# Performance work log

Hardware: AMD Instinct MI355X
Metric: run time of the kernel (lower is better)

Reference implementation:

```python
import jax, jax.numpy as jnp
import numpy as np

N_NODES = 50000
N_EDGES = 600000
IN_DIM = 128
HID = 256
N_CLASSES = 16


def setup_inputs() -> dict:
    key = jax.random.key(0)
    ks = jax.random.split(key, 10)
    x = jax.random.normal(ks[0], (N_NODES, IN_DIM), dtype=jnp.float32)
    edge_index = jax.random.randint(ks[1], (2, N_EDGES), 0, N_NODES, dtype=jnp.int64)

    def lin(k, fan_in, fan_out):
        return jax.random.normal(k, (fan_in, fan_out), dtype=jnp.float32) / np.sqrt(fan_in)

    return {
        "x": x,
        "edge_index": edge_index,
        # SAGEConv1: lin_l acts on aggregated neighbors (has bias), lin_r on root (no bias)
        "w1_l": lin(ks[2], IN_DIM, HID),
        "b1_l": jnp.zeros((HID,), dtype=jnp.float32),
        "w1_r": lin(ks[3], IN_DIM, HID),
        # SAGEConv2
        "w2_l": lin(ks[4], HID, HID),
        "b2_l": jnp.zeros((HID,), dtype=jnp.float32),
        "w2_r": lin(ks[5], HID, HID),
        # classifier
        "wc": lin(ks[6], HID, N_CLASSES),
        "bc": jnp.zeros((N_CLASSES,), dtype=jnp.float32),
    }


def _sage_conv(x, src, dst, w_l, b_l, w_r):
    """PyG SAGEConv with mean aggregation: lin_l(mean_neigh) + lin_r(x)."""
    n = x.shape[0]
    # scatter-add messages from src nodes into dst nodes  [N, F]
    msg_sum = jax.ops.segment_sum(x[src], dst, num_segments=n)
    deg = jax.ops.segment_sum(jnp.ones_like(dst, dtype=x.dtype), dst, num_segments=n)
    neigh_mean = msg_sum / jnp.maximum(deg, 1.0)[:, None]
    return neigh_mean @ w_l + b_l + x @ w_r


def reference(x, edge_index, w1_l, b1_l, w1_r, w2_l, b2_l, w2_r, wc, bc):
    src, dst = edge_index[0], edge_index[1]
    h = jax.nn.relu(_sage_conv(x, src, dst, w1_l, b1_l, w1_r))
    h = jax.nn.relu(_sage_conv(h, src, dst, w2_l, b2_l, w2_r))
    # dropout is identity in eval mode
    return h @ wc + bc
```

## Files before the change

### kernel.cpp

```cpp
#include <hip/hip_runtime.h>
#include <hip/hip_bf16.h>

typedef unsigned short u16;
typedef __attribute__((ext_vector_type(8))) short s16x8;
typedef __attribute__((ext_vector_type(4))) float f32x4;

#define GLOAD16(src, dst)                                                   \
  __builtin_amdgcn_global_load_lds(                                         \
      (const __attribute__((address_space(1))) void*)(src),                 \
      (__attribute__((address_space(3))) void*)(dst), 16, 0, 0)

__device__ inline u16 f2bf(float f) {
  unsigned u = __float_as_uint(f);
  unsigned r = u + 0x7FFFu + ((u >> 16) & 1u);
  return (u16)(r >> 16);
}
__device__ inline float bf2f(u16 h) { return __uint_as_float(((unsigned)h) << 16); }
__device__ inline void split_hl(float f, u16& hi, u16& lo) {
  hi = f2bf(f);
  lo = f2bf(f - bf2f(hi));
}

__global__ void k_hist(const int* __restrict__ dst, int* __restrict__ deg, int nE) {
  int i = blockIdx.x * blockDim.x + threadIdx.x;
  if (i < nE) atomicAdd(&deg[dst[i]], 1);
}

__global__ void k_scan_chunks(const int* __restrict__ deg, int* __restrict__ excl,
                              int* __restrict__ partials, int n) {
  __shared__ int sd[256];
  const int t = threadIdx.x;
  const int base = blockIdx.x * 1024 + t * 4;
  int v0 = (base + 0 < n) ? deg[base + 0] : 0;
  int v1 = (base + 1 < n) ? deg[base + 1] : 0;
  int v2 = (base + 2 < n) ? deg[base + 2] : 0;
  int v3 = (base + 3 < n) ? deg[base + 3] : 0;
  sd[t] = v0 + v1 + v2 + v3;
  __syncthreads();
  for (int off = 1; off < 256; off <<= 1) {
    int x = 0;
    if (t >= off) x = sd[t - off];
    __syncthreads();
    sd[t] += x;
    __syncthreads();
  }
  int run = (t > 0) ? sd[t - 1] : 0;
  if (base + 0 < n) excl[base + 0] = run;
  run += v0;
  if (base + 1 < n) excl[base + 1] = run;
  run += v1;
  if (base + 2 < n) excl[base + 2] = run;
  run += v2;
  if (base + 3 < n) excl[base + 3] = run;
  if (t == 255) partials[blockIdx.x] = sd[255];
}

__global__ void k_scan_partials(int* __restrict__ partials, int nchunk) {
  const int t = threadIdx.x;
  int orig = (t < nchunk) ? partials[t] : 0;
  int v = orig;
  for (int off = 1; off < 64; off <<= 1) {
    int y = __shfl_up(v, off, 64);
    if (t >= off) v += y;
  }
  if (t < nchunk) partials[t] = v - orig;
}

__global__ void k_add_offsets(int* __restrict__ rowstart, const int* __restrict__ chunk_off,
                              int n, int nE) {
  int i = blockIdx.x * blockDim.x + threadIdx.x;
  if (i < n) rowstart[i] += chunk_off[i >> 10];
  if (i == n) rowstart[n] = nE;
}

__global__ void k_fill(const int* __restrict__ src, const int* __restrict__ dst,
                       const int* __restrict__ rowstart, int* __restrict__ cursor,
                       int* __restrict__ csr, int nE) {
  int i = blockIdx.x * blockDim.x + threadIdx.x;
  if (i < nE) {
    int d = dst[i];
    int p = rowstart[d] + atomicAdd(&cursor[d], 1);
    csr[p] = src[i];
  }
}

__global__ void k_cvt(const float* __restrict__ X, u16* __restrict__ hi,
                      u16* __restrict__ lo, long n) {
  long i = (long)(blockIdx.x * blockDim.x + threadIdx.x) * 4;
  if (i >= n) return;
  float4 v = *(const float4*)&X[i];
  u16 h0, l0, h1, l1, h2, l2, h3, l3;
  split_hl(v.x, h0, l0);
  split_hl(v.y, h1, l1);
  split_hl(v.z, h2, l2);
  split_hl(v.w, h3, l3);
  *(ushort4*)&hi[i] = make_ushort4(h0, h1, h2, h3);
  *(ushort4*)&lo[i] = make_ushort4(l0, l1, l2, l3);
}

__global__ void k_cvt_wt(const float* __restrict__ W, u16* __restrict__ thi,
                         u16* __restrict__ tlo, int K, int N) {
  int i = blockIdx.x * blockDim.x + threadIdx.x;
  if (i >= K * N) return;
  int k = i / N, n = i - k * N;
  u16 h, l;
  split_hl(W[i], h, l);
  thi[n * K + k] = h;
  tlo[n * K + k] = l;
}

__global__ void k_agg128_hl(const float* __restrict__ X, const int* __restrict__ rs,
                            const int* __restrict__ csr, u16* __restrict__ ohi,
                            u16* __restrict__ olo, int M) {
  int wid = (blockIdx.x * blockDim.x + threadIdx.x) >> 6;
  int lane = threadIdx.x & 63;
  if (wid >= M) return;
  int s0 = rs[wid], s1 = rs[wid + 1];
  float ax = 0.f, ay = 0.f;
  int e = s0;
  for (; e + 1 < s1; e += 2) {
    int sa = csr[e], sb = csr[e + 1];
    float2 va = *(const float2*)&X[(size_t)sa * 128 + lane * 2];
    float2 vb = *(const float2*)&X[(size_t)sb * 128 + lane * 2];
    ax += va.x + vb.x;
    ay += va.y + vb.y;
  }
  if (e < s1) {
    float2 va = *(const float2*)&X[(size_t)csr[e] * 128 + lane * 2];
    ax += va.x;
    ay += va.y;
  }
  float inv = 1.0f / fmaxf((float)(s1 - s0), 1.0f);
  ax *= inv;
  ay *= inv;
  u16 h0, l0, h1, l1;
  split_hl(ax, h0, l0);
  split_hl(ay, h1, l1);
  size_t o = (size_t)wid * 128 + lane * 2;
  *(ushort2*)&ohi[o] = make_ushort2(h0, h1);
  *(ushort2*)&olo[o] = make_ushort2(l0, l1);
}

__global__ void k_agg256_hl(const u16* __restrict__ Xhi, const u16* __restrict__ Xlo,
                            const int* __restrict__ rs, const int* __restrict__ csr,
                            u16* __restrict__ ohi, u16* __restrict__ olo, int M) {
  int wid = (blockIdx.x * blockDim.x + threadIdx.x) >> 6;
  int lane = threadIdx.x & 63;
  if (wid >= M) return;
  int s0 = rs[wid], s1 = rs[wid + 1];
  float a0 = 0.f, a1 = 0.f, a2 = 0.f, a3 = 0.f;
  int e = s0;
  for (; e + 1 < s1; e += 2) {
    size_t ba = (size_t)csr[e] * 256 + lane * 4;
    size_t bb = (size_t)csr[e + 1] * 256 + lane * 4;
    ushort4 ha = *(const ushort4*)&Xhi[ba];
    ushort4 la = *(const ushort4*)&Xlo[ba];
    ushort4 hb = *(const ushort4*)&Xhi[bb];
    ushort4 lb = *(const ushort4*)&Xlo[bb];
    a0 += bf2f(ha.x) + bf2f(la.x) + bf2f(hb.x) + bf2f(lb.x);
    a1 += bf2f(ha.y) + bf2f(la.y) + bf2f(hb.y) + bf2f(lb.y);
    a2 += bf2f(ha.z) + bf2f(la.z) + bf2f(hb.z) + bf2f(lb.z);
    a3 += bf2f(ha.w) + bf2f(la.w) + bf2f(hb.w) + bf2f(lb.w);
  }
  if (e < s1) {
    size_t ba = (size_t)csr[e] * 256 + lane * 4;
    ushort4 ha = *(const ushort4*)&Xhi[ba];
    ushort4 la = *(const ushort4*)&Xlo[ba];
    a0 += bf2f(ha.x) + bf2f(la.x);
    a1 += bf2f(ha.y) + bf2f(la.y);
    a2 += bf2f(ha.z) + bf2f(la.z);
    a3 += bf2f(ha.w) + bf2f(la.w);
  }
  float inv = 1.0f / fmaxf((float)(s1 - s0), 1.0f);
  a0 *= inv;
  a1 *= inv;
  a2 *= inv;
  a3 *= inv;
  u16 h0, l0, h1, l1, h2, l2, h3, l3;
  split_hl(a0, h0, l0);
  split_hl(a1, h1, l1);
  split_hl(a2, h2, l2);
  split_hl(a3, h3, l3);
  size_t o = (size_t)wid * 256 + lane * 4;
  *(ushort4*)&ohi[o] = make_ushort4(h0, h1, h2, h3);
  *(ushort4*)&olo[o] = make_ushort4(l0, l1, l2, l3);
}

template <int OUT_HL>
__global__ __launch_bounds__(256) void k_gemm_mfma(
    const u16* __restrict__ A1h, const u16* __restrict__ A1l,
    const u16* __restrict__ A2h, const u16* __restrict__ A2l,
    const u16* __restrict__ W1h, const u16* __restrict__ W1l,
    const u16* __restrict__ W2h, const u16* __restrict__ W2l,
    const float* __restrict__ bias, u16* __restrict__ Ohi, u16* __restrict__ Olo,
    float* __restrict__ Of32, int M, int K) {
  __shared__ short sAh[2][4096], sAl[2][4096], sBh[2][4096], sBl[2][4096];
  const int t = threadIdx.x;
  const int l = t & 63;
  const int w = t >> 6;
  const int wr = w >> 1, wc = w & 1;
  const int bm0 = blockIdx.x * 128;
  const int bn0 = blockIdx.y * 128;
  const int NT = (2 * K) / 32;

  f32x4 acc[4][4];
#pragma unroll
  for (int m = 0; m < 4; m++)
#pragma unroll
    for (int n = 0; n < 4; n++) acc[m][n] = (f32x4){0.f, 0.f, 0.f, 0.f};

  const int s0 = t, s1 = 256 + t;
  const int kg0 = s0 >> 7, r0 = s0 & 127;
  const int kg1 = s1 >> 7, r1 = s1 & 127;

#define STAGE(buf, it)                                                        \
  do {                                                                        \
    int kk_ = (it) * 32;                                                      \
    int ph_ = kk_ >= K;                                                       \
    int kb_ = kk_ - (ph_ ? K : 0);                                            \
    const u16* Ah_ = ph_ ? A2h : A1h;                                         \
    const u16* Al_ = ph_ ? A2l : A1l;                                         \
    const u16* Bh_ = ph_ ? W2h : W1h;                                         \
    const u16* Bl_ = ph_ ? W2l : W1l;                                         \
    size_t a0_ = (size_t)(bm0 + r0) * K + kb_ + kg0 * 8;                      \
    size_t a1_ = (size_t)(bm0 + r1) * K + kb_ + kg1 * 8;                      \
    size_t b0_ = (size_t)(bn0 + r0) * K + kb_ + kg0 * 8;                      \
    size_t b1_ = (size_t)(bn0 + r1) * K + kb_ + kg1 * 8;                      \
    GLOAD16(Ah_ + a0_, &sAh[buf][s0 * 8]);                                    \
    GLOAD16(Ah_ + a1_, &sAh[buf][s1 * 8]);                                    \
    GLOAD16(Al_ + a0_, &sAl[buf][s0 * 8]);                                    \
    GLOAD16(Al_ + a1_, &sAl[buf][s1 * 8]);                                    \
    GLOAD16(Bh_ + b0_, &sBh[buf][s0 * 8]);                                    \
    GLOAD16(Bh_ + b1_, &sBh[buf][s1 * 8]);                                    \
    GLOAD16(Bl_ + b0_, &sBl[buf][s0 * 8]);                                    \
    GLOAD16(Bl_ + b1_, &sBl[buf][s1 * 8]);                                    \
  } while (0)

  STAGE(0, 0);
  STAGE(1, 1);

  const int kg = l >> 4;
  const int lr = l & 15;
  for (int it = 0; it < NT; ++it) {
    const int buf = it & 1;
    if (it + 1 < NT) {
      asm volatile("s_waitcnt vmcnt(8)" ::: "memory");
    } else {
      asm volatile("s_waitcnt vmcnt(0)" ::: "memory");
    }
    __builtin_amdgcn_s_barrier();

    s16x8 ah[4], al[4], bh[4], bl[4];
#pragma unroll
    for (int m = 0; m < 4; ++m) {
      int ao = kg * 1024 + (wr * 64 + m * 16 + lr) * 8;
      ah[m] = *(const s16x8*)&sAh[buf][ao];
      al[m] = *(const s16x8*)&sAl[buf][ao];
    }
#pragma unroll
    for (int n = 0; n < 4; ++n) {
      int bo = kg * 1024 + (wc * 64 + n * 16 + lr) * 8;
      bh[n] = *(const s16x8*)&sBh[buf][bo];
      bl[n] = *(const s16x8*)&sBl[buf][bo];
    }
    asm volatile("s_waitcnt lgkmcnt(0)" ::: "memory");
    __builtin_amdgcn_s_barrier();
    if (it + 2 < NT) STAGE(buf, it + 2);

#pragma unroll
    for (int n = 0; n < 4; ++n) {
#pragma unroll
      for (int m = 0; m < 4; ++m) {
        acc[m][n] = __builtin_amdgcn_mfma_f32_16x16x32_bf16(ah[m], bh[n], acc[m][n], 0, 0, 0);
        acc[m][n] = __builtin_amdgcn_mfma_f32_16x16x32_bf16(al[m], bh[n], acc[m][n], 0, 0, 0);
        acc[m][n] = __builtin_amdgcn_mfma_f32_16x16x32_bf16(ah[m], bl[n], acc[m][n], 0, 0, 0);
      }
    }
  }
#undef STAGE

  const int colb = bn0 + wc * 64 + lr;
  const int rwb = bm0 + wr * 64 + (l >> 4) * 4;
#pragma unroll
  for (int n = 0; n < 4; ++n) {
    int col = colb + n * 16;
    float bc = bias[col];
#pragma unroll
    for (int m = 0; m < 4; ++m) {
#pragma unroll
      for (int j = 0; j < 4; ++j) {
        int r = rwb + m * 16 + j;
        if (r < M) {
          float v = fmaxf(acc[m][n][j] + bc, 0.f);
          if (OUT_HL) {
            u16 h, lo2;
            split_hl(v, h, lo2);
            Ohi[(size_t)r * 256 + col] = h;
            Olo[(size_t)r * 256 + col] = lo2;
          } else {
            Of32[(size_t)r * 256 + col] = v;
          }
        }
      }
    }
  }
}

__global__ void k_classifier(const float* __restrict__ h2, const float* __restrict__ wc,
                             const float* __restrict__ bc, float* __restrict__ outv, int M) {
  __shared__ float wcs[4096];
  __shared__ float bcs[16];
  const int t = threadIdx.x;
  for (int i = t; i < 4096; i += 256) wcs[i] = wc[i];
  if (t < 16) bcs[t] = bc[t];
  __syncthreads();
  int row = blockIdx.x * 16 + (t >> 4);
  int cls = t & 15;
  if (row >= M) return;
  const float* hr = h2 + (size_t)row * 256;
  float acc = 0.f;
  for (int k = 0; k < 256; k += 4) {
    float4 h = *(const float4*)&hr[k];
    acc += h.x * wcs[(k + 0) * 16 + cls];
    acc += h.y * wcs[(k + 1) * 16 + cls];
    acc += h.z * wcs[(k + 2) * 16 + cls];
    acc += h.w * wcs[(k + 3) * 16 + cls];
  }
  outv[(size_t)row * 16 + cls] = acc + bcs[cls];
}

extern "C" void kernel_launch(void* const* d_in, const int* in_sizes, int n_in,
                              void* d_out, int out_size, void* d_ws, size_t ws_size,
                              hipStream_t stream) {
  const float* x = (const float*)d_in[0];
  const int* ei = (const int*)d_in[1];
  const float* w1l = (const float*)d_in[2];
  const float* b1l = (const float*)d_in[3];
  const float* w1r = (const float*)d_in[4];
  const float* w2l = (const float*)d_in[5];
  const float* b2l = (const float*)d_in[6];
  const float* w2r = (const float*)d_in[7];
  const float* wc = (const float*)d_in[8];
  const float* bc = (const float*)d_in[9];
  float* outp = (float*)d_out;

  const int nE = in_sizes[1] / 2;
  const int M = in_sizes[0] / 128;
  const int Mpad = (M + 127) & ~127;
  const int* src = ei;
  const int* dst = ei + nE;

  char* ws = (char*)d_ws;
  const size_t SZ_P128 = (size_t)Mpad * 128 * 2;
  const size_t SZ_P256 = (size_t)Mpad * 256 * 2;

  int* deg = (int*)(ws + 0);
  int* cursor = (int*)(ws + 262144);
  int* rowstart = (int*)(ws + 524288);
  int* partials = (int*)(ws + 786432);
  int* csr = (int*)(ws + 1048576);
  u16* wt1l_h = (u16*)(ws + 3670016);
  u16* wt1l_l = (u16*)(ws + 3735552);
  u16* wt1r_h = (u16*)(ws + 3801088);
  u16* wt1r_l = (u16*)(ws + 3866624);
  u16* wt2l_h = (u16*)(ws + 3932160);
  u16* wt2l_l = (u16*)(ws + 4063232);
  u16* wt2r_h = (u16*)(ws + 4194304);
  u16* wt2r_l = (u16*)(ws + 4325376);
  char* big = ws + 4718592;
  u16* x_hi = (u16*)(big);
  u16* x_lo = (u16*)(big + SZ_P128);
  u16* n1_hi = (u16*)(big + 2 * SZ_P128);
  u16* n1_lo = (u16*)(big + 3 * SZ_P128);
  float* h2 = (float*)(big);
  char* big2 = big + 4 * SZ_P128;
  u16* h1_hi = (u16*)(big2);
  u16* h1_lo = (u16*)(big2 + SZ_P256);
  u16* n2_hi = (u16*)(big2 + 2 * SZ_P256);
  u16* n2_lo = (u16*)(big2 + 3 * SZ_P256);

  hipMemsetAsync(deg, 0, (size_t)M * sizeof(int), stream);
  hipMemsetAsync(cursor, 0, (size_t)M * sizeof(int), stream);

  const int eb = (nE + 255) / 256;
  k_hist<<<eb, 256, 0, stream>>>(dst, deg, nE);
  const int nchunk = (M + 1023) / 1024;
  k_scan_chunks<<<nchunk, 256, 0, stream>>>(deg, rowstart, partials, M);
  k_scan_partials<<<1, 64, 0, stream>>>(partials, nchunk);
  k_add_offsets<<<(M + 1 + 255) / 256, 256, 0, stream>>>(rowstart, partials, M, nE);
  k_fill<<<eb, 256, 0, stream>>>(src, dst, rowstart, cursor, csr, nE);

  long nx = (long)M * 128;
  k_cvt<<<(int)((nx / 4 + 255) / 256), 256, 0, stream>>>(x, x_hi, x_lo, nx);
  k_cvt_wt<<<(128 * 256 + 255) / 256, 256, 0, stream>>>(w1l, wt1l_h, wt1l_l, 128, 256);
  k_cvt_wt<<<(128 * 256 + 255) / 256, 256, 0, stream>>>(w1r, wt1r_h, wt1r_l, 128, 256);
  k_cvt_wt<<<(256 * 256 + 255) / 256, 256, 0, stream>>>(w2l, wt2l_h, wt2l_l, 256, 256);
  k_cvt_wt<<<(256 * 256 + 255) / 256, 256, 0, stream>>>(w2r, wt2r_h, wt2r_l, 256, 256);

  dim3 ggrid(Mpad / 128, 2);

  k_agg128_hl<<<(M * 64 + 255) / 256, 256, 0, stream>>>(x, rowstart, csr, n1_hi, n1_lo, M);
  k_gemm_mfma<1><<<ggrid, 256, 0, stream>>>(n1_hi, n1_lo, x_hi, x_lo, wt1l_h, wt1l_l,
                                            wt1r_h, wt1r_l, b1l, h1_hi, h1_lo, nullptr,
                                            M, 128);
  k_agg256_hl<<<(M * 64 + 255) / 256, 256, 0, stream>>>(h1_hi, h1_lo, rowstart, csr, n2_hi,
                                                        n2_lo, M);
  k_gemm_mfma<0><<<ggrid, 256, 0, stream>>>(n2_hi, n2_lo, h1_hi, h1_lo, wt2l_h, wt2l_l,
                                            wt2r_h, wt2r_l, b2l, nullptr, nullptr, h2,
                                            M, 256);
  k_classifier<<<(M + 15) / 16, 256, 0, stream>>>(h2, wc, bc, outp, M);
}
```

Measured before the change: 491.9 us.

## Use k-tiled swizzled packed layout and 64x256 GEMM tiles

Activations and weights are stored in a k-major packed layout (32-wide k tiles per node row) with an XOR swizzle, so each GEMM stage loads contiguous 16-byte chunks and LDS reads avoid bank conflicts. The GEMM tile changes from 128x128 with two column blocks to 64 rows by the full 256 columns, with each wave owning 64 columns and sharing the A tile. The aggregation and conversion kernels are updated to read and write the new layout. This costs more LDS for B per block and less A reuse per B load, and the gather in agg256 now touches 32-element strided segments.

```diff
diff --git a/kernel.cpp b/kernel.cpp
--- a/kernel.cpp
+++ b/kernel.cpp
@@ -19,6 +19,11 @@
 __device__ inline void split_hl(float f, u16& hi, u16& lo) {
   hi = f2bf(f);
   lo = f2bf(f - bf2f(hi));
+}
+
+__device__ inline size_t pk_idx(int node, int f, size_t MpadS) {
+  return (size_t)(f >> 5) * MpadS + (size_t)node * 32 +
+         (size_t)(((((f >> 3) & 3) ^ ((node >> 1) & 3)) << 3) + (f & 7));
 }
 
 __global__ void k_hist(const int* __restrict__ dst, int* __restrict__ deg, int nE) {
@@ -85,7 +90,7 @@
 }
 
 __global__ void k_cvt(const float* __restrict__ X, u16* __restrict__ hi,
-                      u16* __restrict__ lo, long n) {
+                      u16* __restrict__ lo, long n, size_t MpadS) {
   long i = (long)(blockIdx.x * blockDim.x + threadIdx.x) * 4;
   if (i >= n) return;
   float4 v = *(const float4*)&X[i];
@@ -94,24 +99,28 @@
   split_hl(v.y, h1, l1);
   split_hl(v.z, h2, l2);
   split_hl(v.w, h3, l3);
-  *(ushort4*)&hi[i] = make_ushort4(h0, h1, h2, h3);
-  *(ushort4*)&lo[i] = make_ushort4(l0, l1, l2, l3);
+  int node = (int)(i >> 7), f = (int)(i & 127);
+  size_t o = pk_idx(node, f, MpadS);
+  *(ushort4*)&hi[o] = make_ushort4(h0, h1, h2, h3);
+  *(ushort4*)&lo[o] = make_ushort4(l0, l1, l2, l3);
 }
 
 __global__ void k_cvt_wt(const float* __restrict__ W, u16* __restrict__ thi,
-                         u16* __restrict__ tlo, int K, int N) {
+                         u16* __restrict__ tlo, int K) {
   int i = blockIdx.x * blockDim.x + threadIdx.x;
-  if (i >= K * N) return;
-  int k = i / N, n = i - k * N;
+  if (i >= K * 256) return;
+  int k = i >> 8, n = i & 255;
   u16 h, l;
   split_hl(W[i], h, l);
-  thi[n * K + k] = h;
-  tlo[n * K + k] = l;
+  size_t o = (size_t)(k >> 5) * 8192 + (size_t)n * 32 +
+             (size_t)(((((k >> 3) & 3) ^ ((n >> 1) & 3)) << 3) + (k & 7));
+  thi[o] = h;
+  tlo[o] = l;
 }
 
 __global__ void k_agg128_hl(const float* __restrict__ X, const int* __restrict__ rs,
                             const int* __restrict__ csr, u16* __restrict__ ohi,
-                            u16* __restrict__ olo, int M) {
+                            u16* __restrict__ olo, int M, size_t MpadS) {
   int wid = (blockIdx.x * blockDim.x + threadIdx.x) >> 6;
   int lane = threadIdx.x & 63;
   if (wid >= M) return;
@@ -136,23 +145,28 @@
   u16 h0, l0, h1, l1;
   split_hl(ax, h0, l0);
   split_hl(ay, h1, l1);
-  size_t o = (size_t)wid * 128 + lane * 2;
+  size_t o = pk_idx(wid, 2 * lane, MpadS);
   *(ushort2*)&ohi[o] = make_ushort2(h0, h1);
   *(ushort2*)&olo[o] = make_ushort2(l0, l1);
 }
 
 __global__ void k_agg256_hl(const u16* __restrict__ Xhi, const u16* __restrict__ Xlo,
                             const int* __restrict__ rs, const int* __restrict__ csr,
-                            u16* __restrict__ ohi, u16* __restrict__ olo, int M) {
+                            u16* __restrict__ ohi, u16* __restrict__ olo, int M,
+                            size_t MpadS) {
   int wid = (blockIdx.x * blockDim.x + threadIdx.x) >> 6;
   int lane = threadIdx.x & 63;
   if (wid >= M) return;
   int s0 = rs[wid], s1 = rs[wid + 1];
+  const size_t ktb = (size_t)(lane >> 3) * MpadS;
+  const int cg = (lane >> 1) & 3;
+  const int off = (lane & 1) * 4;
   float a0 = 0.f, a1 = 0.f, a2 = 0.f, a3 = 0.f;
   int e = s0;
   for (; e + 1 < s1; e += 2) {
-    size_t ba = (size_t)csr[e] * 256 + lane * 4;
-    size_t bb = (size_t)csr[e + 1] * 256 + lane * 4;
+    int na = csr[e], nb = csr[e + 1];
+    size_t ba = ktb + (size_t)na * 32 + ((cg ^ ((na >> 1) & 3)) << 3) + off;
+    size_t bb = ktb + (size_t)nb * 32 + ((cg ^ ((nb >> 1) & 3)) << 3) + off;
     ushort4 ha = *(const ushort4*)&Xhi[ba];
     ushort4 la = *(const ushort4*)&Xlo[ba];
     ushort4 hb = *(const ushort4*)&Xhi[bb];
@@ -163,7 +177,8 @@
     a3 += bf2f(ha.w) + bf2f(la.w) + bf2f(hb.w) + bf2f(lb.w);
   }
   if (e < s1) {
-    size_t ba = (size_t)csr[e] * 256 + lane * 4;
+    int na = csr[e];
+    size_t ba = ktb + (size_t)na * 32 + ((cg ^ ((na >> 1) & 3)) << 3) + off;
     ushort4 ha = *(const ushort4*)&Xhi[ba];
     ushort4 la = *(const ushort4*)&Xlo[ba];
     a0 += bf2f(ha.x) + bf2f(la.x);
@@ -181,7 +196,7 @@
   split_hl(a1, h1, l1);
   split_hl(a2, h2, l2);
   split_hl(a3, h3, l3);
-  size_t o = (size_t)wid * 256 + lane * 4;
+  size_t o = ktb + (size_t)wid * 32 + ((cg ^ ((wid >> 1) & 3)) << 3) + off;
   *(ushort4*)&ohi[o] = make_ushort4(h0, h1, h2, h3);
   *(ushort4*)&olo[o] = make_ushort4(l0, l1, l2, l3);
 }
@@ -193,58 +208,54 @@
     const u16* __restrict__ W1h, const u16* __restrict__ W1l,
     const u16* __restrict__ W2h, const u16* __restrict__ W2l,
     const float* __restrict__ bias, u16* __restrict__ Ohi, u16* __restrict__ Olo,
-    float* __restrict__ Of32, int M, int K) {
-  __shared__ short sAh[2][4096], sAl[2][4096], sBh[2][4096], sBl[2][4096];
+    float* __restrict__ Of32, int M, int K, size_t MpadS) {
+  __shared__ short sAh[2][2048], sAl[2][2048], sBh[2][8192], sBl[2][8192];
   const int t = threadIdx.x;
   const int l = t & 63;
   const int w = t >> 6;
-  const int wr = w >> 1, wc = w & 1;
-  const int bm0 = blockIdx.x * 128;
-  const int bn0 = blockIdx.y * 128;
-  const int NT = (2 * K) / 32;
+  const int bm0 = blockIdx.x * 64;
+  const int KT = K >> 5;
+  const int NT = 2 * KT;
 
   f32x4 acc[4][4];
 #pragma unroll
   for (int m = 0; m < 4; m++)
 #pragma unroll
     for (int n = 0; n < 4; n++) acc[m][n] = (f32x4){0.f, 0.f, 0.f, 0.f};
-
-  const int s0 = t, s1 = 256 + t;
-  const int kg0 = s0 >> 7, r0 = s0 & 127;
-  const int kg1 = s1 >> 7, r1 = s1 & 127;
 
 #define STAGE(buf, it)                                                        \
   do {                                                                        \
-    int kk_ = (it) * 32;                                                      \
-    int ph_ = kk_ >= K;                                                       \
-    int kb_ = kk_ - (ph_ ? K : 0);                                            \
+    int ph_ = (it) >= KT;                                                     \
+    int kt_ = (it) - (ph_ ? KT : 0);                                          \
     const u16* Ah_ = ph_ ? A2h : A1h;                                         \
     const u16* Al_ = ph_ ? A2l : A1l;                                         \
     const u16* Bh_ = ph_ ? W2h : W1h;                                         \
     const u16* Bl_ = ph_ ? W2l : W1l;                                         \
-    size_t a0_ = (size_t)(bm0 + r0) * K + kb_ + kg0 * 8;                      \
-    size_t a1_ = (size_t)(bm0 + r1) * K + kb_ + kg1 * 8;                      \
-    size_t b0_ = (size_t)(bn0 + r0) * K + kb_ + kg0 * 8;                      \
-    size_t b1_ = (size_t)(bn0 + r1) * K + kb_ + kg1 * 8;                      \
-    GLOAD16(Ah_ + a0_, &sAh[buf][s0 * 8]);                                    \
-    GLOAD16(Ah_ + a1_, &sAh[buf][s1 * 8]);                                    \
-    GLOAD16(Al_ + a0_, &sAl[buf][s0 * 8]);                                    \
-    GLOAD16(Al_ + a1_, &sAl[buf][s1 * 8]);                                    \
-    GLOAD16(Bh_ + b0_, &sBh[buf][s0 * 8]);                                    \
-    GLOAD16(Bh_ + b1_, &sBh[buf][s1 * 8]);                                    \
-    GLOAD16(Bl_ + b0_, &sBl[buf][s0 * 8]);                                    \
-    GLOAD16(Bl_ + b1_, &sBl[buf][s1 * 8]);                                    \
+    size_t ab_ = (size_t)kt_ * MpadS + (size_t)bm0 * 32 + t * 8;              \
+    size_t bb_ = (size_t)kt_ * 8192 + t * 8;                                  \
+    GLOAD16(Ah_ + ab_, &sAh[buf][t * 8]);                                     \
+    GLOAD16(Al_ + ab_, &sAl[buf][t * 8]);                                     \
+    GLOAD16(Bh_ + bb_ + 0 * 2048, &sBh[buf][t * 8 + 0 * 2048]);               \
+    GLOAD16(Bh_ + bb_ + 1 * 2048, &sBh[buf][t * 8 + 1 * 2048]);               \
+    GLOAD16(Bh_ + bb_ + 2 * 2048, &sBh[buf][t * 8 + 2 * 2048]);               \
+    GLOAD16(Bh_ + bb_ + 3 * 2048, &sBh[buf][t * 8 + 3 * 2048]);               \
+    GLOAD16(Bl_ + bb_ + 0 * 2048, &sBl[buf][t * 8 + 0 * 2048]);               \
+    GLOAD16(Bl_ + bb_ + 1 * 2048, &sBl[buf][t * 8 + 1 * 2048]);               \
+    GLOAD16(Bl_ + bb_ + 2 * 2048, &sBl[buf][t * 8 + 2 * 2048]);               \
+    GLOAD16(Bl_ + bb_ + 3 * 2048, &sBl[buf][t * 8 + 3 * 2048]);               \
   } while (0)
 
   STAGE(0, 0);
   STAGE(1, 1);
 
-  const int kg = l >> 4;
   const int lr = l & 15;
+  const int cw = l >> 4;
+  const int csx = ((cw ^ ((lr >> 1) & 3)) << 3);
+
   for (int it = 0; it < NT; ++it) {
     const int buf = it & 1;
     if (it + 1 < NT) {
-      asm volatile("s_waitcnt vmcnt(8)" ::: "memory");
+      asm volatile("s_waitcnt vmcnt(10)" ::: "memory");
     } else {
       asm volatile("s_waitcnt vmcnt(0)" ::: "memory");
     }
@@ -253,17 +264,18 @@
     s16x8 ah[4], al[4], bh[4], bl[4];
 #pragma unroll
     for (int m = 0; m < 4; ++m) {
-      int ao = kg * 1024 + (wr * 64 + m * 16 + lr) * 8;
+      int ao = (m * 16 + lr) * 32 + csx;
       ah[m] = *(const s16x8*)&sAh[buf][ao];
       al[m] = *(const s16x8*)&sAl[buf][ao];
     }
 #pragma unroll
     for (int n = 0; n < 4; ++n) {
-      int bo = kg * 1024 + (wc * 64 + n * 16 + lr) * 8;
+      int bo = (w * 64 + n * 16 + lr) * 32 + csx;
       bh[n] = *(const s16x8*)&sBh[buf][bo];
       bl[n] = *(const s16x8*)&sBl[buf][bo];
     }
     asm volatile("s_waitcnt lgkmcnt(0)" ::: "memory");
+    __builtin_amdgcn_sched_barrier(0);
     __builtin_amdgcn_s_barrier();
     if (it + 2 < NT) STAGE(buf, it + 2);
 
@@ -279,8 +291,8 @@
   }
 #undef STAGE
 
-  const int colb = bn0 + wc * 64 + lr;
-  const int rwb = bm0 + wr * 64 + (l >> 4) * 4;
+  const int colb = w * 64 + lr;
+  const int rwb = bm0 + (l >> 4) * 4;
 #pragma unroll
   for (int n = 0; n < 4; ++n) {
     int col = colb + n * 16;
@@ -295,8 +307,9 @@
           if (OUT_HL) {
             u16 h, lo2;
             split_hl(v, h, lo2);
-            Ohi[(size_t)r * 256 + col] = h;
-            Olo[(size_t)r * 256 + col] = lo2;
+            size_t o = pk_idx(r, col, MpadS);
+            Ohi[o] = h;
+            Olo[o] = lo2;
           } else {
             Of32[(size_t)r * 256 + col] = v;
           }
@@ -346,7 +359,8 @@
 
   const int nE = in_sizes[1] / 2;
   const int M = in_sizes[0] / 128;
-  const int Mpad = (M + 127) & ~127;
+  const int Mpad = (M + 63) & ~63;
+  const size_t MpadS = (size_t)Mpad * 32;
   const int* src = ei;
   const int* dst = ei + nE;
 
@@ -391,22 +405,23 @@
   k_fill<<<eb, 256, 0, stream>>>(src, dst, rowstart, cursor, csr, nE);
 
   long nx = (long)M * 128;
-  k_cvt<<<(int)((nx / 4 + 255) / 256), 256, 0, stream>>>(x, x_hi, x_lo, nx);
-  k_cvt_wt<<<(128 * 256 + 255) / 256, 256, 0, stream>>>(w1l, wt1l_h, wt1l_l, 128, 256);
-  k_cvt_wt<<<(128 * 256 + 255) / 256, 256, 0, stream>>>(w1r, wt1r_h, wt1r_l, 128, 256);
-  k_cvt_wt<<<(256 * 256 + 255) / 256, 256, 0, stream>>>(w2l, wt2l_h, wt2l_l, 256, 256);
-  k_cvt_wt<<<(256 * 256 + 255) / 256, 256, 0, stream>>>(w2r, wt2r_h, wt2r_l, 256, 256);
-
-  dim3 ggrid(Mpad / 128, 2);
-
-  k_agg128_hl<<<(M * 64 + 255) / 256, 256, 0, stream>>>(x, rowstart, csr, n1_hi, n1_lo, M);
+  k_cvt<<<(int)((nx / 4 + 255) / 256), 256, 0, stream>>>(x, x_hi, x_lo, nx, MpadS);
+  k_cvt_wt<<<(128 * 256 + 255) / 256, 256, 0, stream>>>(w1l, wt1l_h, wt1l_l, 128);
+  k_cvt_wt<<<(128 * 256 + 255) / 256, 256, 0, stream>>>(w1r, wt1r_h, wt1r_l, 128);
+  k_cvt_wt<<<(256 * 256 + 255) / 256, 256, 0, stream>>>(w2l, wt2l_h, wt2l_l, 256);
+  k_cvt_wt<<<(256 * 256 + 255) / 256, 256, 0, stream>>>(w2r, wt2r_h, wt2r_l, 256);
+
+  const int ggrid = Mpad / 64;
+
+  k_agg128_hl<<<(M * 64 + 255) / 256, 256, 0, stream>>>(x, rowstart, csr, n1_hi, n1_lo, M,
+                                                        MpadS);
   k_gemm_mfma<1><<<ggrid, 256, 0, stream>>>(n1_hi, n1_lo, x_hi, x_lo, wt1l_h, wt1l_l,
                                             wt1r_h, wt1r_l, b1l, h1_hi, h1_lo, nullptr,
-                                            M, 128);
+                                            M, 128, MpadS);
   k_agg256_hl<<<(M * 64 + 255) / 256, 256, 0, stream>>>(h1_hi, h1_lo, rowstart, csr, n2_hi,
-                                                        n2_lo, M);
+                                                        n2_lo, M, MpadS);
   k_gemm_mfma<0><<<ggrid, 256, 0, stream>>>(n2_hi, n2_lo, h1_hi, h1_lo, wt2l_h, wt2l_l,
                                             wt2r_h, wt2r_l, b2l, nullptr, nullptr, h2,
-                                            M, 256);
+                                            M, 256, MpadS);
   k_classifier<<<(M + 15) / 16, 256, 0, stream>>>(h2, wc, bc, outp, M);
 }
```

Result: slower. 533.3 us (+8.4%).
